# Performance work log

Measured on AMD Instinct MI355X. Metric: run time of the kernel, lower is better.

The kernel has to match this reference:

```python
import jax, jax.numpy as jnp
import numpy as np

B, N, D = 16, 2048, 128
SCALE = 1.0 / np.sqrt(D).astype(np.float32)


def setup_inputs() -> dict:
    key = jax.random.key(0)
    ks = jax.random.split(key, 9)
    Q = jax.random.normal(ks[0], (B, N, D), dtype=jnp.float32)
    K = jax.random.normal(ks[1], (B, N, D), dtype=jnp.float32)
    V = jax.random.normal(ks[2], (B, N, D), dtype=jnp.float32)
    bias_dis = 0.1 * jax.random.normal(ks[3], (N, N), dtype=jnp.float32)
    bias_dtw = 0.1 * jax.random.normal(ks[4], (N, N), dtype=jnp.float32)
    bias_pattern = 0.1 * jax.random.normal(ks[5], (N, N), dtype=jnp.float32)
    bias_poi = 0.1 * jax.random.normal(ks[6], (N, N), dtype=jnp.float32)
    # key/query padding masks: mostly True (valid) with some padding
    input_mask = jax.random.randint(ks[7], (B, N), 0, 10) > 0
    embeddings_mask = jax.random.randint(ks[8], (B, N), 0, 10) > 0
    # lower-triangular causal mask (diagonal kept so every row has a valid key)
    causal_mask = jnp.tril(jnp.ones((N, N), dtype=bool))
    return {"Q": Q, "K": K, "V": V, "bias_dis": bias_dis, "bias_dtw": bias_dtw,
            "bias_pattern": bias_pattern, "bias_poi": bias_poi,
            "input_mask": input_mask, "embeddings_mask": embeddings_mask,
            "causal_mask": causal_mask}


def reference(Q, K, V, bias_dis, bias_dtw, bias_pattern, bias_poi,
              input_mask, embeddings_mask, causal_mask):
    # masked_fill_(~mask, 0.0) on K, V with input_mask[:, :, None]
    km = input_mask[:, :, None]
    K = jnp.where(km, K, 0.0)
    V = jnp.where(km, V, 0.0)
    # masked_fill_(~mask, 0.0) on Q with embeddings_mask[:, :, None]
    Q = jnp.where(embeddings_mask[:, :, None], Q, 0.0)
    # scores [B, N, N] = Q K^T / sqrt(dim)
    scores = jnp.einsum('bnd,bmd->bnm', Q, K) * SCALE
    # causal masked_fill_(~causal_mask, -inf)
    scores = jnp.where(causal_mask[None, :, :], scores, -jnp.inf)
    # per-batch bias loop == broadcast add of summed [N, N] biases
    scores = scores + (bias_dis + bias_dtw + bias_pattern + bias_poi)[None, :, :]
    P = jax.nn.softmax(scores, axis=-1)
    # dropout p=0 (eval) -> identity
    return jnp.einsum('bnm,bmd->bnd', P, V)
```

## Files before the change

kernel.cpp:

```cpp
#include <hip/hip_runtime.h>
#include <math.h>

constexpr int Bc = 16;
constexpr int Nc = 2048;
constexpr int Dc = 128;
constexpr int NCHUNK = Nc / 64;
constexpr float SCALE_F = 0.08838834764831845f;

typedef __bf16 bf16x8 __attribute__((ext_vector_type(8)));
typedef __bf16 bf16x4 __attribute__((ext_vector_type(4)));
typedef float  f32x4  __attribute__((ext_vector_type(4)));

constexpr size_t KPACK_BYTES = (size_t)Bc * NCHUNK * 16 * 64 * 16;
constexpr size_t VPACK_BYTES = KPACK_BYTES;
constexpr int NUNITS = 1056;
constexpr size_t BIASP_BYTES = (size_t)NUNITS * 2048 * 4;
constexpr int CHUNK_ELEMS = 16 * 64 * 8;
constexpr int PART_FLOATS = 64 * 128 + 64 + 64;
constexpr size_t PART_BYTES = (size_t)Bc * 72 * PART_FLOATS * 4;

__device__ __forceinline__ int ftri(int t) {
    const int m = t >> 1;
    return (t & 1) ? (m + 1) * (m + 1) : m * (m + 1);
}

__device__ __forceinline__ void gload_lds16(const __bf16* gsrc, __bf16* ldst) {
    __builtin_amdgcn_global_load_lds(
        (const __attribute__((address_space(1))) unsigned int*)gsrc,
        (__attribute__((address_space(3))) unsigned int*)ldst, 16, 0, 0);
}

template<int CTRL>
__device__ __forceinline__ float dpp_mv(float v) {
    return __builtin_bit_cast(float,
        __builtin_amdgcn_update_dpp(0, __builtin_bit_cast(int, v),
                                    CTRL, 0xF, 0xF, true));
}
__device__ __forceinline__ float rmax16(float v) {
    v = fmaxf(v, dpp_mv<0xB1>(v));
    v = fmaxf(v, dpp_mv<0x4E>(v));
    v = fmaxf(v, dpp_mv<0x141>(v));
    v = fmaxf(v, dpp_mv<0x140>(v));
    return v;
}
__device__ __forceinline__ float rsum16(float v) {
    v += dpp_mv<0xB1>(v);
    v += dpp_mv<0x4E>(v);
    v += dpp_mv<0x141>(v);
    v += dpp_mv<0x140>(v);
    return v;
}

__global__ __launch_bounds__(256) void prep_fused(
    const float* __restrict__ K, const float* __restrict__ V,
    const int* __restrict__ imask,
    const float* __restrict__ b0, const float* __restrict__ b1,
    const float* __restrict__ b2, const float* __restrict__ b3,
    __bf16* __restrict__ Kp, __bf16* __restrict__ Vp, float* __restrict__ bsp)
{
    __shared__ __align__(16) __bf16 Ks[64][136];
    __shared__ __align__(16) __bf16 Vs[64][136];
    __shared__ __align__(16) float  Ts[32][68];
    const int bid = blockIdx.x;
    const int tid = threadIdx.x;

    if (bid >= 512) {
        const int u = bid - 512;
        int t = 0;
        while (ftri(t + 1) <= u) ++t;
        const int c = u - ftri(t);

        #pragma unroll
        for (int i = 0; i < 2; ++i) {
            const int v = tid + 256 * i;
            const int row = v >> 4, c4 = v & 15;
            const size_t g = (size_t)(t * 32 + row) * Nc + c * 64 + c4 * 4;
            const float4 a = *(const float4*)(b0 + g);
            const float4 d = *(const float4*)(b1 + g);
            const float4 e = *(const float4*)(b2 + g);
            const float4 f = *(const float4*)(b3 + g);
            float4 s;
            s.x = a.x + d.x + e.x + f.x;
            s.y = a.y + d.y + e.y + f.y;
            s.z = a.z + d.z + e.z + f.z;
            s.w = a.w + d.w + e.w + f.w;
            *(float4*)&Ts[row][c4 * 4] = s;
        }
        __syncthreads();

        const int lane = tid >> 2;
        const int quad = lane >> 4, l15 = lane & 15;
        const int k0 = (tid & 3) * 8;
        float* outp = bsp + (size_t)u * 2048;
        #pragma unroll
        for (int g2 = 0; g2 < 2; ++g2) {
            const int k = k0 + g2 * 4;
            const int h = (k >> 4) & 1, jt = (k >> 2) & 3;
            float4 o;
            o.x = Ts[h * 16 + quad * 4 + 0][jt * 16 + l15];
            o.y = Ts[h * 16 + quad * 4 + 1][jt * 16 + l15];
            o.z = Ts[h * 16 + quad * 4 + 2][jt * 16 + l15];
            o.w = Ts[h * 16 + quad * 4 + 3][jt * 16 + l15];
            ((float4*)outp)[tid * 2 + g2] = o;
        }
        return;
    }

    const int c = bid & 31;
    const int b = bid >> 5;
    const int m0 = c * 64;
    const float* Kb = K + (size_t)b * Nc * Dc;
    const float* Vb = V + (size_t)b * Nc * Dc;
    const int* imb = imask + b * Nc;

    #pragma unroll
    for (int it = 0; it < 8; ++it) {
        const int idx = it * 256 + tid;
        const int row = idx >> 5;
        const int c4  = idx & 31;
        const int gm  = m0 + row;
        const float msk = imb[gm] ? 1.0f : 0.0f;
        const float4 kf = ((const float4*)(Kb + (size_t)gm * Dc))[c4];
        const float4 vf = ((const float4*)(Vb + (size_t)gm * Dc))[c4];
        bf16x4 kb, vb;
        kb[0] = (__bf16)(kf.x * msk); kb[1] = (__bf16)(kf.y * msk);
        kb[2] = (__bf16)(kf.z * msk); kb[3] = (__bf16)(kf.w * msk);
        vb[0] = (__bf16)(vf.x * msk); vb[1] = (__bf16)(vf.y * msk);
        vb[2] = (__bf16)(vf.z * msk); vb[3] = (__bf16)(vf.w * msk);
        *(bf16x4*)&Ks[row][c4 * 4] = kb;
        *(bf16x4*)&Vs[row][c4 * 4] = vb;
    }
    __syncthreads();

    const size_t chunk_base = (size_t)(b * NCHUNK + c) * CHUNK_ELEMS;
    #pragma unroll
    for (int i = 0; i < 4; ++i) {
        const int s = i * 256 + tid;
        const int f = s >> 6;
        const int l = s & 63;
        const int quad = (l >> 4) & 3;
        const int l15  = l & 15;
        {
            const int jt = f >> 2, kd = f & 3;
            const bf16x8 kv = *(const bf16x8*)&Ks[jt * 16 + l15][kd * 32 + quad * 8];
            *(bf16x8*)&Kp[chunk_base + (size_t)f * 512 + l * 8] = kv;
        }
        {
            const int kj = f >> 3, dt = f & 7;
            bf16x8 vv;
            #pragma unroll
            for (int j = 0; j < 8; ++j)
                vv[j] = Vs[kj * 32 + quad * 8 + j][dt * 16 + l15];
            *(bf16x8*)&Vp[chunk_base + (size_t)f * 512 + l * 8] = vv;
        }
    }
}

template<bool SPLIT>
__global__ __launch_bounds__(256) void attn_pipe2(
    const float* __restrict__ Q,
    const __bf16* __restrict__ Kp, const __bf16* __restrict__ Vp,
    const float* __restrict__ biasp, const int* __restrict__ emask,
    float* __restrict__ out, float* __restrict__ part)
{
    __shared__ __align__(16) __bf16 Kl[2][16 * 512];
    __shared__ __align__(16) __bf16 Vl[2][16 * 512];
    __shared__ __align__(16) __bf16 Pl[4][16][72];

    const int tid  = threadIdx.x;
    const int w    = tid >> 6;
    const int lane = tid & 63;
    const int quad = lane >> 4;
    const int l15  = lane & 15;
    const int b = blockIdx.x;

    int t, c0, cend, pidx;
    bool direct;
    if (SPLIT) {
        const int u = 79 - blockIdx.y;
        int s;
        if (u < 8)       { t = u;                 s = 0; }
        else if (u < 24) { t = 8  + ((u - 8) >> 1);  s = (u - 8) & 1; }
        else if (u < 48) { t = 16 + (u - 24) / 3;    s = (u - 24) % 3; }
        else             { t = 24 + ((u - 48) >> 2); s = (u - 48) & 3; }
        c0 = s * 8;
        cend = min(t + 1, c0 + 8);
        direct = (u < 8);
        pidx = u - 8;
    } else {
        const int y = blockIdx.y;
        t = (y < 16) ? y : (47 - y);
        c0 = 0; cend = t + 1; direct = true; pidx = 0;
    }

    const int q0w = t * 64 + w * 16;
    const int t32 = t * 2 + (w >> 1);
    const int hh  = w & 1;
    const int fb32 = ftri(t32);

    const float*  Qb  = Q + (size_t)b * Nc * Dc;
    const __bf16* Kpb = Kp + (size_t)b * NCHUNK * CHUNK_ELEMS;
    const __bf16* Vpb = Vp + (size_t)b * NCHUNK * CHUNK_ELEMS;
    const f32x4* bfrag = (const f32x4*)biasp + (size_t)lane * 8 + hh * 4;

    bf16x8 qfrag[4];
    {
        const int row = q0w + l15;
        const float qs = emask[b * Nc + row] ? SCALE_F : 0.0f;
        const float4* qr = (const float4*)(Qb + (size_t)row * Dc);
        #pragma unroll
        for (int kd = 0; kd < 4; ++kd) {
            const float4 xx = qr[kd * 8 + quad * 2];
            const float4 yy = qr[kd * 8 + quad * 2 + 1];
            qfrag[kd][0] = (__bf16)(xx.x * qs); qfrag[kd][1] = (__bf16)(xx.y * qs);
            qfrag[kd][2] = (__bf16)(xx.z * qs); qfrag[kd][3] = (__bf16)(xx.w * qs);
            qfrag[kd][4] = (__bf16)(yy.x * qs); qfrag[kd][5] = (__bf16)(yy.y * qs);
            qfrag[kd][6] = (__bf16)(yy.z * qs); qfrag[kd][7] = (__bf16)(yy.w * qs);
        }
    }

    f32x4 oacc[8];
    #pragma unroll
    for (int dt = 0; dt < 8; ++dt) { oacc[dt][0]=0.f; oacc[dt][1]=0.f; oacc[dt][2]=0.f; oacc[dt][3]=0.f; }
    float mrun[4] = {-INFINITY, -INFINITY, -INFINITY, -INFINITY};
    float lrun[4] = {0.f, 0.f, 0.f, 0.f};

    const int nch = cend - c0;

    #pragma unroll
    for (int i = 0; i < 4; ++i) {
        const int seg = w * 4 + i;
        gload_lds16(Kpb + (size_t)c0 * CHUNK_ELEMS + seg * 512 + lane * 8, &Kl[0][seg * 512]);
        gload_lds16(Vpb + (size_t)c0 * CHUNK_ELEMS + seg * 512 + lane * 8, &Vl[0][seg * 512]);
    }
    f32x4 binit[4];
    #pragma unroll
    for (int jt = 0; jt < 4; ++jt)
        binit[jt] = bfrag[(size_t)(fb32 + c0) * 512 + jt];
    __syncthreads();

    f32x4 sc[4];
    #pragma unroll
    for (int jt = 0; jt < 4; ++jt) sc[jt] = binit[jt];
    #pragma unroll
    for (int jt = 0; jt < 4; ++jt)
        #pragma unroll
        for (int kd = 0; kd < 4; ++kd) {
            const bf16x8 bfr = *(const bf16x8*)&Kl[0][(jt * 4 + kd) * 512 + lane * 8];
            sc[jt] = __builtin_amdgcn_mfma_f32_16x16x32_bf16(qfrag[kd], bfr, sc[jt], 0, 0, 0);
        }
    if (nch > 1) {
        #pragma unroll
        for (int i = 0; i < 4; ++i) {
            const int seg = w * 4 + i;
            gload_lds16(Kpb + (size_t)(c0 + 1) * CHUNK_ELEMS + seg * 512 + lane * 8, &Kl[1][seg * 512]);
            gload_lds16(Vpb + (size_t)(c0 + 1) * CHUNK_ELEMS + seg * 512 + lane * 8, &Vl[1][seg * 512]);
        }
        #pragma unroll
        for (int jt = 0; jt < 4; ++jt)
            binit[jt] = bfrag[(size_t)(fb32 + c0 + 1) * 512 + jt];
    }

    for (int c = c0; c < cend; ++c) {
        const int cb = (c - c0) & 1;

        if (c == t) {
            const int m0 = c * 64;
            #pragma unroll
            for (int jt = 0; jt < 4; ++jt)
                #pragma unroll
                for (int reg = 0; reg < 4; ++reg) {
                    const int gr = q0w + quad * 4 + reg;
                    const int gc = m0 + jt * 16 + l15;
                    if (gc > gr) sc[jt][reg] = -INFINITY;
                }
        }

        #pragma unroll
        for (int reg = 0; reg < 4; ++reg) {
            float mx = fmaxf(fmaxf(sc[0][reg], sc[1][reg]), fmaxf(sc[2][reg], sc[3][reg]));
            mx = rmax16(mx);
            const float mn = fmaxf(mrun[reg], mx);
            const float alpha = __expf(mrun[reg] - mn);
            mrun[reg] = mn;
            lrun[reg] *= alpha;
            #pragma unroll
            for (int dt = 0; dt < 8; ++dt) oacc[dt][reg] *= alpha;
            float ls = 0.f;
            #pragma unroll
            for (int jt = 0; jt < 4; ++jt) {
                const float pv = __expf(sc[jt][reg] - mn);
                sc[jt][reg] = pv;
                ls += pv;
            }
            lrun[reg] += rsum16(ls);
        }

        #pragma unroll
        for (int jt = 0; jt < 4; ++jt)
            #pragma unroll
            for (int reg = 0; reg < 4; ++reg)
                Pl[w][quad * 4 + reg][jt * 16 + l15] = (__bf16)sc[jt][reg];

        #pragma unroll
        for (int kj = 0; kj < 2; ++kj) {
            const bf16x8 pa = *(const bf16x8*)&Pl[w][l15][kj * 32 + quad * 8];
            #pragma unroll
            for (int dt = 0; dt < 8; ++dt) {
                const bf16x8 vb = *(const bf16x8*)&Vl[cb][(kj * 8 + dt) * 512 + lane * 8];
                oacc[dt] = __builtin_amdgcn_mfma_f32_16x16x32_bf16(pa, vb, oacc[dt], 0, 0, 0);
            }
        }

        __syncthreads();

        const bool n1 = (c + 1) < cend;
        const bool n2 = (c + 2) < cend;

        if (n2) {
            const size_t off = (size_t)(c + 2) * CHUNK_ELEMS;
            #pragma unroll
            for (int i = 0; i < 4; ++i) {
                const int seg = w * 4 + i;
                gload_lds16(Kpb + off + seg * 512 + lane * 8, &Kl[cb][seg * 512]);
                gload_lds16(Vpb + off + seg * 512 + lane * 8, &Vl[cb][seg * 512]);
            }
        }

        if (n1) {
            #pragma unroll
            for (int jt = 0; jt < 4; ++jt) sc[jt] = binit[jt];
            #pragma unroll
            for (int jt = 0; jt < 4; ++jt)
                #pragma unroll
                for (int kd = 0; kd < 4; ++kd) {
                    const bf16x8 bfr = *(const bf16x8*)&Kl[cb ^ 1][(jt * 4 + kd) * 512 + lane * 8];
                    sc[jt] = __builtin_amdgcn_mfma_f32_16x16x32_bf16(qfrag[kd], bfr, sc[jt], 0, 0, 0);
                }
        }
        if (n2) {
            #pragma unroll
            for (int jt = 0; jt < 4; ++jt)
                binit[jt] = bfrag[(size_t)(fb32 + c + 2) * 512 + jt];
        }
    }

    if (direct) {
        #pragma unroll
        for (int reg = 0; reg < 4; ++reg) {
            const float inv = 1.0f / lrun[reg];
            const int gr = q0w + quad * 4 + reg;
            float* orow = out + ((size_t)b * Nc + gr) * Dc;
            #pragma unroll
            for (int dt = 0; dt < 8; ++dt)
                orow[dt * 16 + l15] = oacc[dt][reg] * inv;
        }
    } else {
        float* pb = part + (size_t)(b * 72 + pidx) * PART_FLOATS;
        #pragma unroll
        for (int reg = 0; reg < 4; ++reg) {
            const int lr = w * 16 + quad * 4 + reg;
            #pragma unroll
            for (int dt = 0; dt < 8; ++dt)
                pb[lr * 128 + dt * 16 + l15] = oacc[dt][reg];
            if (l15 == 0) {
                pb[8192 + lr] = mrun[reg];
                pb[8256 + lr] = lrun[reg];
            }
        }
    }
}

__global__ __launch_bounds__(256) void merge_parts(
    const float* __restrict__ part, float* __restrict__ out)
{
    const int b = blockIdx.x;
    const int t = 8 + blockIdx.y;
    const int S = (t < 16) ? 2 : ((t < 24) ? 3 : 4);
    const int pbase = (t < 16) ? 2 * (t - 8)
                    : (t < 24) ? 16 + 3 * (t - 16)
                               : 40 + 4 * (t - 24);
    const int r  = threadIdx.x >> 2;
    const int cq = threadIdx.x & 3;
    const float* p0 = part + (size_t)(b * 72 + pbase) * PART_FLOATS;

    float m[4], a[4];
    float mstar = -INFINITY;
    #pragma unroll
    for (int s = 0; s < 4; ++s)
        if (s < S) { m[s] = p0[(size_t)s * PART_FLOATS + 8192 + r]; mstar = fmaxf(mstar, m[s]); }
    float lsum = 0.f;
    #pragma unroll
    for (int s = 0; s < 4; ++s)
        if (s < S) {
            a[s] = __expf(m[s] - mstar);
            lsum += p0[(size_t)s * PART_FLOATS + 8256 + r] * a[s];
        }
    const float inv = 1.0f / lsum;

    float* orow = out + ((size_t)b * Nc + t * 64 + r) * Dc + cq * 32;
    #pragma unroll
    for (int i = 0; i < 8; ++i) {
        float x = 0.f, y = 0.f, z = 0.f, ww = 0.f;
        #pragma unroll
        for (int s = 0; s < 4; ++s)
            if (s < S) {
                const f32x4 v = *(const f32x4*)&p0[(size_t)s * PART_FLOATS + r * 128 + cq * 32 + i * 4];
                x += v[0] * a[s]; y += v[1] * a[s]; z += v[2] * a[s]; ww += v[3] * a[s];
            }
        f32x4 o; o[0] = x * inv; o[1] = y * inv; o[2] = z * inv; o[3] = ww * inv;
        *(f32x4*)&orow[i * 4] = o;
    }
}

__global__ __launch_bounds__(256) void attn_mfma_legacy(
    const float* __restrict__ Q, const float* __restrict__ K, const float* __restrict__ V,
    const float* __restrict__ p0, const float* __restrict__ p1,
    const float* __restrict__ p2, const float* __restrict__ p3,
    const int* __restrict__ imask, const int* __restrict__ emask,
    float* __restrict__ out)
{
    __shared__ __align__(16) __bf16 Klds[64][136];
    __shared__ __align__(16) __bf16 Vt[128][72];
    __shared__ __align__(16) __bf16 Plds[4][16][72];
    const int tid  = threadIdx.x;
    const int w    = tid >> 6;
    const int lane = tid & 63;
    const int quad = lane >> 4;
    const int l15  = lane & 15;
    const int b = blockIdx.y;
    const int x = blockIdx.x, yy = blockIdx.y;
    const int ti = (yy < 8) ? x : (31 - x);
    const int q0 = ti * 64, q0w = q0 + w * 16;
    const float* Qb = Q + (size_t)b * Nc * Dc;
    const float* Kb = K + (size_t)b * Nc * Dc;
    const float* Vb = V + (size_t)b * Nc * Dc;
    const int* imb = imask + b * Nc;

    bf16x8 qfrag[4];
    {
        const int row = q0w + l15;
        const float qs = emask[b * Nc + row] ? SCALE_F : 0.0f;
        const float4* qr = (const float4*)(Qb + (size_t)row * Dc);
        #pragma unroll
        for (int kd = 0; kd < 4; ++kd) {
            const float4 xv = qr[kd * 8 + quad * 2];
            const float4 yv = qr[kd * 8 + quad * 2 + 1];
            qfrag[kd][0]=(__bf16)(xv.x*qs); qfrag[kd][1]=(__bf16)(xv.y*qs);
            qfrag[kd][2]=(__bf16)(xv.z*qs); qfrag[kd][3]=(__bf16)(xv.w*qs);
            qfrag[kd][4]=(__bf16)(yv.x*qs); qfrag[kd][5]=(__bf16)(yv.y*qs);
            qfrag[kd][6]=(__bf16)(yv.z*qs); qfrag[kd][7]=(__bf16)(yv.w*qs);
        }
    }
    f32x4 oacc[8];
    #pragma unroll
    for (int dt = 0; dt < 8; ++dt){oacc[dt][0]=0.f;oacc[dt][1]=0.f;oacc[dt][2]=0.f;oacc[dt][3]=0.f;}
    float mrun[4]={-INFINITY,-INFINITY,-INFINITY,-INFINITY}, lrun[4]={0.f,0.f,0.f,0.f};

    for (int m0 = 0; m0 <= q0; m0 += 64) {
        __syncthreads();
        #pragma unroll
        for (int it = 0; it < 8; ++it) {
            const int idx = it * 256 + tid;
            const int row = idx >> 5, c4 = idx & 31;
            const int gm = m0 + row;
            const float msk = imb[gm] ? 1.0f : 0.0f;
            const float4 kf = ((const float4*)(Kb + (size_t)gm * Dc))[c4];
            const float4 vf = ((const float4*)(Vb + (size_t)gm * Dc))[c4];
            bf16x4 kb;
            kb[0]=(__bf16)(kf.x*msk); kb[1]=(__bf16)(kf.y*msk);
            kb[2]=(__bf16)(kf.z*msk); kb[3]=(__bf16)(kf.w*msk);
            *(bf16x4*)&Klds[row][c4*4] = kb;
            Vt[c4*4+0][row]=(__bf16)(vf.x*msk); Vt[c4*4+1][row]=(__bf16)(vf.y*msk);
            Vt[c4*4+2][row]=(__bf16)(vf.z*msk); Vt[c4*4+3][row]=(__bf16)(vf.w*msk);
        }
        __syncthreads();
        f32x4 sc[4];
        #pragma unroll
        for (int jt = 0; jt < 4; ++jt){sc[jt][0]=0.f;sc[jt][1]=0.f;sc[jt][2]=0.f;sc[jt][3]=0.f;}
        #pragma unroll
        for (int jt = 0; jt < 4; ++jt)
            #pragma unroll
            for (int kd = 0; kd < 4; ++kd) {
                const bf16x8 bfr = *(const bf16x8*)&Klds[jt*16+l15][kd*32+quad*8];
                sc[jt] = __builtin_amdgcn_mfma_f32_16x16x32_bf16(qfrag[kd], bfr, sc[jt], 0, 0, 0);
            }
        #pragma unroll
        for (int jt = 0; jt < 4; ++jt)
            #pragma unroll
            for (int reg = 0; reg < 4; ++reg) {
                const int gr = q0w + quad*4 + reg;
                const int gc = m0 + jt*16 + l15;
                const size_t boff = (size_t)gr * Nc + gc;
                const float bsx = p0[boff] + p1[boff] + p2[boff] + p3[boff];
                const float v = sc[jt][reg] + bsx;
                sc[jt][reg] = (gc > gr) ? -INFINITY : v;
            }
        #pragma unroll
        for (int reg = 0; reg < 4; ++reg) {
            float mx = fmaxf(fmaxf(sc[0][reg], sc[1][reg]), fmaxf(sc[2][reg], sc[3][reg]));
            mx = rmax16(mx);
            const float mn = fmaxf(mrun[reg], mx);
            const float alpha = __expf(mrun[reg] - mn);
            mrun[reg] = mn; lrun[reg] *= alpha;
            #pragma unroll
            for (int dt = 0; dt < 8; ++dt) oacc[dt][reg] *= alpha;
            float ls = 0.f;
            #pragma unroll
            for (int jt = 0; jt < 4; ++jt) {
                const float pv = __expf(sc[jt][reg] - mn);
                sc[jt][reg] = pv; ls += pv;
            }
            lrun[reg] += rsum16(ls);
        }
        #pragma unroll
        for (int jt = 0; jt < 4; ++jt)
            #pragma unroll
            for (int reg = 0; reg < 4; ++reg)
                Plds[w][quad*4+reg][jt*16+l15] = (__bf16)sc[jt][reg];
        #pragma unroll
        for (int kj = 0; kj < 2; ++kj) {
            const bf16x8 pa = *(const bf16x8*)&Plds[w][l15][kj*32+quad*8];
            #pragma unroll
            for (int dt = 0; dt < 8; ++dt) {
                const bf16x8 vb = *(const bf16x8*)&Vt[dt*16+l15][kj*32+quad*8];
                oacc[dt] = __builtin_amdgcn_mfma_f32_16x16x32_bf16(pa, vb, oacc[dt], 0, 0, 0);
            }
        }
    }
    #pragma unroll
    for (int reg = 0; reg < 4; ++reg) {
        const float inv = 1.0f / lrun[reg];
        const int gr = q0w + quad*4 + reg;
        float* orow = out + ((size_t)b * Nc + gr) * Dc;
        #pragma unroll
        for (int dt = 0; dt < 8; ++dt)
            orow[dt*16+l15] = oacc[dt][reg] * inv;
    }
}

extern "C" void kernel_launch(void* const* d_in, const int* in_sizes, int n_in,
                              void* d_out, int out_size, void* d_ws, size_t ws_size,
                              hipStream_t stream) {
    const float* Q  = (const float*)d_in[0];
    const float* K  = (const float*)d_in[1];
    const float* V  = (const float*)d_in[2];
    const float* b0 = (const float*)d_in[3];
    const float* b1 = (const float*)d_in[4];
    const float* b2 = (const float*)d_in[5];
    const float* b3 = (const float*)d_in[6];
    const int* im   = (const int*)d_in[7];
    const int* em   = (const int*)d_in[8];
    float* out      = (float*)d_out;

    const size_t need_full  = KPACK_BYTES + VPACK_BYTES + BIASP_BYTES;
    const size_t need_split = need_full + PART_BYTES;

    if (ws_size >= need_full) {
        __bf16* Kp  = (__bf16*)d_ws;
        __bf16* Vp  = (__bf16*)((char*)d_ws + KPACK_BYTES);
        float*  bsp = (float*)((char*)d_ws + KPACK_BYTES + VPACK_BYTES);
        float*  prt = (float*)((char*)d_ws + need_full);
        prep_fused<<<512 + NUNITS, 256, 0, stream>>>(
            K, V, im, b0, b1, b2, b3, Kp, Vp, bsp);
        if (ws_size >= need_split) {
            attn_pipe2<true><<<dim3(Bc, 80), 256, 0, stream>>>(
                Q, Kp, Vp, bsp, em, out, prt);
            merge_parts<<<dim3(Bc, 24), 256, 0, stream>>>(prt, out);
        } else {
            attn_pipe2<false><<<dim3(Bc, 32), 256, 0, stream>>>(
                Q, Kp, Vp, bsp, em, out, nullptr);
        }
    } else {
        attn_mfma_legacy<<<dim3(NCHUNK, Bc), 256, 0, stream>>>(
            Q, K, V, b0, b1, b2, b3, im, em, out);
    }
}
```

Measured before the change: 240.3 us.

## Load V fragments directly from global into registers and skip non-growing rescale

```diff
diff --git a/kernel.cpp b/kernel.cpp
--- a/kernel.cpp
+++ b/kernel.cpp
@@ -157,14 +157,13 @@
 }
 
 template<bool SPLIT>
-__global__ __launch_bounds__(256) void attn_pipe2(
+__global__ __launch_bounds__(256) void attn_pipe3(
     const float* __restrict__ Q,
     const __bf16* __restrict__ Kp, const __bf16* __restrict__ Vp,
     const float* __restrict__ biasp, const int* __restrict__ emask,
     float* __restrict__ out, float* __restrict__ part)
 {
     __shared__ __align__(16) __bf16 Kl[2][16 * 512];
-    __shared__ __align__(16) __bf16 Vl[2][16 * 512];
     __shared__ __align__(16) __bf16 Pl[4][16][72];
 
     const int tid  = threadIdx.x;
@@ -231,7 +230,6 @@
     for (int i = 0; i < 4; ++i) {
         const int seg = w * 4 + i;
         gload_lds16(Kpb + (size_t)c0 * CHUNK_ELEMS + seg * 512 + lane * 8, &Kl[0][seg * 512]);
-        gload_lds16(Vpb + (size_t)c0 * CHUNK_ELEMS + seg * 512 + lane * 8, &Vl[0][seg * 512]);
     }
     f32x4 binit[4];
     #pragma unroll
@@ -254,7 +252,6 @@
         for (int i = 0; i < 4; ++i) {
             const int seg = w * 4 + i;
             gload_lds16(Kpb + (size_t)(c0 + 1) * CHUNK_ELEMS + seg * 512 + lane * 8, &Kl[1][seg * 512]);
-            gload_lds16(Vpb + (size_t)(c0 + 1) * CHUNK_ELEMS + seg * 512 + lane * 8, &Vl[1][seg * 512]);
         }
         #pragma unroll
         for (int jt = 0; jt < 4; ++jt)
@@ -263,6 +260,12 @@
 
     for (int c = c0; c < cend; ++c) {
         const int cb = (c - c0) & 1;
+        const __bf16* vc = Vpb + (size_t)c * CHUNK_ELEMS;
+
+        bf16x8 va[8];
+        #pragma unroll
+        for (int dt = 0; dt < 8; ++dt)
+            va[dt] = *(const bf16x8*)&vc[(size_t)dt * 512 + lane * 8];
 
         if (c == t) {
             const int m0 = c * 64;
@@ -276,20 +279,32 @@
                 }
         }
 
+        float mx[4];
+        int grow = 0;
         #pragma unroll
         for (int reg = 0; reg < 4; ++reg) {
-            float mx = fmaxf(fmaxf(sc[0][reg], sc[1][reg]), fmaxf(sc[2][reg], sc[3][reg]));
-            mx = rmax16(mx);
-            const float mn = fmaxf(mrun[reg], mx);
-            const float alpha = __expf(mrun[reg] - mn);
-            mrun[reg] = mn;
-            lrun[reg] *= alpha;
-            #pragma unroll
-            for (int dt = 0; dt < 8; ++dt) oacc[dt][reg] *= alpha;
+            float m = fmaxf(fmaxf(sc[0][reg], sc[1][reg]), fmaxf(sc[2][reg], sc[3][reg]));
+            m = rmax16(m);
+            mx[reg] = m;
+            grow |= (m > mrun[reg]);
+        }
+        if (__any(grow)) {
+            #pragma unroll
+            for (int reg = 0; reg < 4; ++reg) {
+                const float mn = fmaxf(mrun[reg], mx[reg]);
+                const float alpha = __expf(mrun[reg] - mn);
+                mrun[reg] = mn;
+                lrun[reg] *= alpha;
+                #pragma unroll
+                for (int dt = 0; dt < 8; ++dt) oacc[dt][reg] *= alpha;
+            }
+        }
+        #pragma unroll
+        for (int reg = 0; reg < 4; ++reg) {
             float ls = 0.f;
             #pragma unroll
             for (int jt = 0; jt < 4; ++jt) {
-                const float pv = __expf(sc[jt][reg] - mn);
+                const float pv = __expf(sc[jt][reg] - mrun[reg]);
                 sc[jt][reg] = pv;
                 ls += pv;
             }
@@ -302,14 +317,20 @@
             for (int reg = 0; reg < 4; ++reg)
                 Pl[w][quad * 4 + reg][jt * 16 + l15] = (__bf16)sc[jt][reg];
 
-        #pragma unroll
-        for (int kj = 0; kj < 2; ++kj) {
-            const bf16x8 pa = *(const bf16x8*)&Pl[w][l15][kj * 32 + quad * 8];
-            #pragma unroll
-            for (int dt = 0; dt < 8; ++dt) {
-                const bf16x8 vb = *(const bf16x8*)&Vl[cb][(kj * 8 + dt) * 512 + lane * 8];
-                oacc[dt] = __builtin_amdgcn_mfma_f32_16x16x32_bf16(pa, vb, oacc[dt], 0, 0, 0);
-            }
+        bf16x8 vb8[8];
+        #pragma unroll
+        for (int dt = 0; dt < 8; ++dt)
+            vb8[dt] = *(const bf16x8*)&vc[(size_t)(8 + dt) * 512 + lane * 8];
+
+        {
+            const bf16x8 pa0 = *(const bf16x8*)&Pl[w][l15][quad * 8];
+            #pragma unroll
+            for (int dt = 0; dt < 8; ++dt)
+                oacc[dt] = __builtin_amdgcn_mfma_f32_16x16x32_bf16(pa0, va[dt], oacc[dt], 0, 0, 0);
+            const bf16x8 pa1 = *(const bf16x8*)&Pl[w][l15][32 + quad * 8];
+            #pragma unroll
+            for (int dt = 0; dt < 8; ++dt)
+                oacc[dt] = __builtin_amdgcn_mfma_f32_16x16x32_bf16(pa1, vb8[dt], oacc[dt], 0, 0, 0);
         }
 
         __syncthreads();
@@ -323,7 +344,6 @@
             for (int i = 0; i < 4; ++i) {
                 const int seg = w * 4 + i;
                 gload_lds16(Kpb + off + seg * 512 + lane * 8, &Kl[cb][seg * 512]);
-                gload_lds16(Vpb + off + seg * 512 + lane * 8, &Vl[cb][seg * 512]);
             }
         }
 
@@ -564,11 +584,11 @@
         prep_fused<<<512 + NUNITS, 256, 0, stream>>>(
             K, V, im, b0, b1, b2, b3, Kp, Vp, bsp);
         if (ws_size >= need_split) {
-            attn_pipe2<true><<<dim3(Bc, 80), 256, 0, stream>>>(
+            attn_pipe3<true><<<dim3(Bc, 80), 256, 0, stream>>>(
                 Q, Kp, Vp, bsp, em, out, prt);
             merge_parts<<<dim3(Bc, 24), 256, 0, stream>>>(prt, out);
         } else {
-            attn_pipe2<false><<<dim3(Bc, 32), 256, 0, stream>>>(
+            attn_pipe3<false><<<dim3(Bc, 32), 256, 0, stream>>>(
                 Q, Kp, Vp, bsp, em, out, nullptr);
         }
     } else {
```

Result: slower. 247.8 us (+3.1%).

## Pack split attention units into balanced persistent slots and skip rescale when max unchanged

Applied to the files above, without the earlier changes.

```diff
diff --git a/kernel.cpp b/kernel.cpp
--- a/kernel.cpp
+++ b/kernel.cpp
@@ -18,6 +18,17 @@
 constexpr int CHUNK_ELEMS = 16 * 64 * 8;
 constexpr int PART_FLOATS = 64 * 128 + 64 + 64;
 constexpr size_t PART_BYTES = (size_t)Bc * 72 * PART_FLOATS * 4;
+
+__device__ __constant__ int SLOT_UNITS[32][3] = {
+    { 7,  6,  1}, { 8, 21, 11}, {10, 44, 29}, {12, 75, 55},
+    {14,  5,  2}, {16, 19, 13}, {18, 41, 32}, {20, 71, 59},
+    {22,  4,  3}, {23, 17, 15}, {24, 38, 35}, {25, 67, 63},
+    {27, 28,  0}, {30, 31,  9}, {33, 34, 26}, {36, 37, 51},
+    {39, 40, -1}, {42, 43, -1}, {45, 46, -1}, {47, 48, -1},
+    {49, 50, -1}, {52, 53, -1}, {54, 56, -1}, {57, 58, -1},
+    {60, 61, -1}, {62, 64, -1}, {65, 66, -1}, {68, 69, -1},
+    {70, 72, -1}, {73, 74, -1}, {76, 77, -1}, {78, 79, -1}
+};
 
 __device__ __forceinline__ int ftri(int t) {
     const int m = t >> 1;
@@ -157,7 +168,7 @@
 }
 
 template<bool SPLIT>
-__global__ __launch_bounds__(256) void attn_pipe2(
+__global__ __launch_bounds__(256) void attn_persist(
     const float* __restrict__ Q,
     const __bf16* __restrict__ Kp, const __bf16* __restrict__ Vp,
     const float* __restrict__ biasp, const int* __restrict__ emask,
@@ -172,200 +183,214 @@
     const int lane = tid & 63;
     const int quad = lane >> 4;
     const int l15  = lane & 15;
-    const int b = blockIdx.x;
-
-    int t, c0, cend, pidx;
-    bool direct;
-    if (SPLIT) {
-        const int u = 79 - blockIdx.y;
-        int s;
-        if (u < 8)       { t = u;                 s = 0; }
-        else if (u < 24) { t = 8  + ((u - 8) >> 1);  s = (u - 8) & 1; }
-        else if (u < 48) { t = 16 + (u - 24) / 3;    s = (u - 24) % 3; }
-        else             { t = 24 + ((u - 48) >> 2); s = (u - 48) & 3; }
-        c0 = s * 8;
-        cend = min(t + 1, c0 + 8);
-        direct = (u < 8);
-        pidx = u - 8;
-    } else {
-        const int y = blockIdx.y;
-        t = (y < 16) ? y : (47 - y);
-        c0 = 0; cend = t + 1; direct = true; pidx = 0;
-    }
-
-    const int q0w = t * 64 + w * 16;
-    const int t32 = t * 2 + (w >> 1);
-    const int hh  = w & 1;
-    const int fb32 = ftri(t32);
+    const int b    = blockIdx.x;
+    const int slot = blockIdx.y;
 
     const float*  Qb  = Q + (size_t)b * Nc * Dc;
     const __bf16* Kpb = Kp + (size_t)b * NCHUNK * CHUNK_ELEMS;
     const __bf16* Vpb = Vp + (size_t)b * NCHUNK * CHUNK_ELEMS;
-    const f32x4* bfrag = (const f32x4*)biasp + (size_t)lane * 8 + hh * 4;
-
-    bf16x8 qfrag[4];
-    {
-        const int row = q0w + l15;
-        const float qs = emask[b * Nc + row] ? SCALE_F : 0.0f;
-        const float4* qr = (const float4*)(Qb + (size_t)row * Dc);
-        #pragma unroll
-        for (int kd = 0; kd < 4; ++kd) {
-            const float4 xx = qr[kd * 8 + quad * 2];
-            const float4 yy = qr[kd * 8 + quad * 2 + 1];
-            qfrag[kd][0] = (__bf16)(xx.x * qs); qfrag[kd][1] = (__bf16)(xx.y * qs);
-            qfrag[kd][2] = (__bf16)(xx.z * qs); qfrag[kd][3] = (__bf16)(xx.w * qs);
-            qfrag[kd][4] = (__bf16)(yy.x * qs); qfrag[kd][5] = (__bf16)(yy.y * qs);
-            qfrag[kd][6] = (__bf16)(yy.z * qs); qfrag[kd][7] = (__bf16)(yy.w * qs);
-        }
-    }
-
-    f32x4 oacc[8];
-    #pragma unroll
-    for (int dt = 0; dt < 8; ++dt) { oacc[dt][0]=0.f; oacc[dt][1]=0.f; oacc[dt][2]=0.f; oacc[dt][3]=0.f; }
-    float mrun[4] = {-INFINITY, -INFINITY, -INFINITY, -INFINITY};
-    float lrun[4] = {0.f, 0.f, 0.f, 0.f};
-
-    const int nch = cend - c0;
-
-    #pragma unroll
-    for (int i = 0; i < 4; ++i) {
-        const int seg = w * 4 + i;
-        gload_lds16(Kpb + (size_t)c0 * CHUNK_ELEMS + seg * 512 + lane * 8, &Kl[0][seg * 512]);
-        gload_lds16(Vpb + (size_t)c0 * CHUNK_ELEMS + seg * 512 + lane * 8, &Vl[0][seg * 512]);
-    }
-    f32x4 binit[4];
-    #pragma unroll
-    for (int jt = 0; jt < 4; ++jt)
-        binit[jt] = bfrag[(size_t)(fb32 + c0) * 512 + jt];
-    __syncthreads();
-
-    f32x4 sc[4];
-    #pragma unroll
-    for (int jt = 0; jt < 4; ++jt) sc[jt] = binit[jt];
-    #pragma unroll
-    for (int jt = 0; jt < 4; ++jt)
-        #pragma unroll
-        for (int kd = 0; kd < 4; ++kd) {
-            const bf16x8 bfr = *(const bf16x8*)&Kl[0][(jt * 4 + kd) * 512 + lane * 8];
-            sc[jt] = __builtin_amdgcn_mfma_f32_16x16x32_bf16(qfrag[kd], bfr, sc[jt], 0, 0, 0);
-        }
-    if (nch > 1) {
+    const f32x4* bfragbase = (const f32x4*)biasp + (size_t)lane * 8 + (w & 1) * 4;
+
+    for (int j = 0; j < 3; ++j) {
+        int t, c0, cend, pidx;
+        bool direct;
+        if (SPLIT) {
+            const int un = SLOT_UNITS[slot][j];
+            if (un < 0) break;
+            if (un < 8)       { t = un;                  c0 = 0; }
+            else if (un < 24) { t = 8  + ((un -  8) >> 1); c0 = ((un -  8) & 1) * 8; }
+            else if (un < 48) { t = 16 + (un - 24) / 3;    c0 = ((un - 24) % 3) * 8; }
+            else              { t = 24 + ((un - 48) >> 2); c0 = ((un - 48) & 3) * 8; }
+            cend = min(t + 1, c0 + 8);
+            direct = (un < 8);
+            pidx = un - 8;
+        } else {
+            if (j) break;
+            t = (slot < 16) ? slot : (47 - slot);
+            c0 = 0; cend = t + 1; direct = true; pidx = 0;
+        }
+
+        const int q0w = t * 64 + w * 16;
+        const int t32 = t * 2 + (w >> 1);
+        const int fb32 = ftri(t32);
+        const f32x4* bfrag = bfragbase;
+
+        bf16x8 qfrag[4];
+        {
+            const int row = q0w + l15;
+            const float qs = emask[b * Nc + row] ? SCALE_F : 0.0f;
+            const float4* qr = (const float4*)(Qb + (size_t)row * Dc);
+            #pragma unroll
+            for (int kd = 0; kd < 4; ++kd) {
+                const float4 xx = qr[kd * 8 + quad * 2];
+                const float4 yy = qr[kd * 8 + quad * 2 + 1];
+                qfrag[kd][0] = (__bf16)(xx.x * qs); qfrag[kd][1] = (__bf16)(xx.y * qs);
+                qfrag[kd][2] = (__bf16)(xx.z * qs); qfrag[kd][3] = (__bf16)(xx.w * qs);
+                qfrag[kd][4] = (__bf16)(yy.x * qs); qfrag[kd][5] = (__bf16)(yy.y * qs);
+                qfrag[kd][6] = (__bf16)(yy.z * qs); qfrag[kd][7] = (__bf16)(yy.w * qs);
+            }
+        }
+
+        f32x4 oacc[8];
+        #pragma unroll
+        for (int dt = 0; dt < 8; ++dt) { oacc[dt][0]=0.f; oacc[dt][1]=0.f; oacc[dt][2]=0.f; oacc[dt][3]=0.f; }
+        float mrun[4] = {-INFINITY, -INFINITY, -INFINITY, -INFINITY};
+        float lrun[4] = {0.f, 0.f, 0.f, 0.f};
+
+        const int nch = cend - c0;
+
         #pragma unroll
         for (int i = 0; i < 4; ++i) {
             const int seg = w * 4 + i;
-            gload_lds16(Kpb + (size_t)(c0 + 1) * CHUNK_ELEMS + seg * 512 + lane * 8, &Kl[1][seg * 512]);
-            gload_lds16(Vpb + (size_t)(c0 + 1) * CHUNK_ELEMS + seg * 512 + lane * 8, &Vl[1][seg * 512]);
-        }
+            gload_lds16(Kpb + (size_t)c0 * CHUNK_ELEMS + seg * 512 + lane * 8, &Kl[0][seg * 512]);
+            gload_lds16(Vpb + (size_t)c0 * CHUNK_ELEMS + seg * 512 + lane * 8, &Vl[0][seg * 512]);
+        }
+        f32x4 binit[4];
         #pragma unroll
         for (int jt = 0; jt < 4; ++jt)
-            binit[jt] = bfrag[(size_t)(fb32 + c0 + 1) * 512 + jt];
-    }
-
-    for (int c = c0; c < cend; ++c) {
-        const int cb = (c - c0) & 1;
-
-        if (c == t) {
-            const int m0 = c * 64;
-            #pragma unroll
-            for (int jt = 0; jt < 4; ++jt)
-                #pragma unroll
-                for (int reg = 0; reg < 4; ++reg) {
-                    const int gr = q0w + quad * 4 + reg;
-                    const int gc = m0 + jt * 16 + l15;
-                    if (gc > gr) sc[jt][reg] = -INFINITY;
-                }
-        }
-
-        #pragma unroll
-        for (int reg = 0; reg < 4; ++reg) {
-            float mx = fmaxf(fmaxf(sc[0][reg], sc[1][reg]), fmaxf(sc[2][reg], sc[3][reg]));
-            mx = rmax16(mx);
-            const float mn = fmaxf(mrun[reg], mx);
-            const float alpha = __expf(mrun[reg] - mn);
-            mrun[reg] = mn;
-            lrun[reg] *= alpha;
-            #pragma unroll
-            for (int dt = 0; dt < 8; ++dt) oacc[dt][reg] *= alpha;
-            float ls = 0.f;
-            #pragma unroll
-            for (int jt = 0; jt < 4; ++jt) {
-                const float pv = __expf(sc[jt][reg] - mn);
-                sc[jt][reg] = pv;
-                ls += pv;
-            }
-            lrun[reg] += rsum16(ls);
-        }
-
+            binit[jt] = bfrag[(size_t)(fb32 + c0) * 512 + jt];
+        __syncthreads();
+
+        f32x4 sc[4];
+        #pragma unroll
+        for (int jt = 0; jt < 4; ++jt) sc[jt] = binit[jt];
         #pragma unroll
         for (int jt = 0; jt < 4; ++jt)
             #pragma unroll
-            for (int reg = 0; reg < 4; ++reg)
-                Pl[w][quad * 4 + reg][jt * 16 + l15] = (__bf16)sc[jt][reg];
-
-        #pragma unroll
-        for (int kj = 0; kj < 2; ++kj) {
-            const bf16x8 pa = *(const bf16x8*)&Pl[w][l15][kj * 32 + quad * 8];
-            #pragma unroll
-            for (int dt = 0; dt < 8; ++dt) {
-                const bf16x8 vb = *(const bf16x8*)&Vl[cb][(kj * 8 + dt) * 512 + lane * 8];
-                oacc[dt] = __builtin_amdgcn_mfma_f32_16x16x32_bf16(pa, vb, oacc[dt], 0, 0, 0);
-            }
-        }
-
-        __syncthreads();
-
-        const bool n1 = (c + 1) < cend;
-        const bool n2 = (c + 2) < cend;
-
-        if (n2) {
-            const size_t off = (size_t)(c + 2) * CHUNK_ELEMS;
+            for (int kd = 0; kd < 4; ++kd) {
+                const bf16x8 bfr = *(const bf16x8*)&Kl[0][(jt * 4 + kd) * 512 + lane * 8];
+                sc[jt] = __builtin_amdgcn_mfma_f32_16x16x32_bf16(qfrag[kd], bfr, sc[jt], 0, 0, 0);
+            }
+        if (nch > 1) {
             #pragma unroll
             for (int i = 0; i < 4; ++i) {
                 const int seg = w * 4 + i;
-                gload_lds16(Kpb + off + seg * 512 + lane * 8, &Kl[cb][seg * 512]);
-                gload_lds16(Vpb + off + seg * 512 + lane * 8, &Vl[cb][seg * 512]);
-            }
-        }
-
-        if (n1) {
-            #pragma unroll
-            for (int jt = 0; jt < 4; ++jt) sc[jt] = binit[jt];
+                gload_lds16(Kpb + (size_t)(c0 + 1) * CHUNK_ELEMS + seg * 512 + lane * 8, &Kl[1][seg * 512]);
+                gload_lds16(Vpb + (size_t)(c0 + 1) * CHUNK_ELEMS + seg * 512 + lane * 8, &Vl[1][seg * 512]);
+            }
             #pragma unroll
             for (int jt = 0; jt < 4; ++jt)
-                #pragma unroll
-                for (int kd = 0; kd < 4; ++kd) {
-                    const bf16x8 bfr = *(const bf16x8*)&Kl[cb ^ 1][(jt * 4 + kd) * 512 + lane * 8];
-                    sc[jt] = __builtin_amdgcn_mfma_f32_16x16x32_bf16(qfrag[kd], bfr, sc[jt], 0, 0, 0);
+                binit[jt] = bfrag[(size_t)(fb32 + c0 + 1) * 512 + jt];
+        }
+
+        for (int c = c0; c < cend; ++c) {
+            const int cb = (c - c0) & 1;
+
+            if (c == t) {
+                const int m0 = c * 64;
+                #pragma unroll
+                for (int jt = 0; jt < 4; ++jt)
+                    #pragma unroll
+                    for (int reg = 0; reg < 4; ++reg) {
+                        const int gr = q0w + quad * 4 + reg;
+                        const int gc = m0 + jt * 16 + l15;
+                        if (gc > gr) sc[jt][reg] = -INFINITY;
+                    }
+            }
+
+            float mx[4];
+            int grow = 0;
+            #pragma unroll
+            for (int reg = 0; reg < 4; ++reg) {
+                float m = fmaxf(fmaxf(sc[0][reg], sc[1][reg]), fmaxf(sc[2][reg], sc[3][reg]));
+                m = rmax16(m);
+                mx[reg] = m;
+                grow |= (m > mrun[reg]);
+            }
+            if (__any(grow)) {
+                #pragma unroll
+                for (int reg = 0; reg < 4; ++reg) {
+                    const float mn = fmaxf(mrun[reg], mx[reg]);
+                    const float alpha = __expf(mrun[reg] - mn);
+                    mrun[reg] = mn;
+                    lrun[reg] *= alpha;
+                    #pragma unroll
+                    for (int dt = 0; dt < 8; ++dt) oacc[dt][reg] *= alpha;
                 }
-        }
-        if (n2) {
+            }
+            #pragma unroll
+            for (int reg = 0; reg < 4; ++reg) {
+                float ls = 0.f;
+                #pragma unroll
+                for (int jt = 0; jt < 4; ++jt) {
+                    const float pv = __expf(sc[jt][reg] - mrun[reg]);
+                    sc[jt][reg] = pv;
+                    ls += pv;
+                }
+                lrun[reg] += rsum16(ls);
+            }
+
             #pragma unroll
             for (int jt = 0; jt < 4; ++jt)
-                binit[jt] = bfrag[(size_t)(fb32 + c + 2) * 512 + jt];
-        }
-    }
-
-    if (direct) {
-        #pragma unroll
-        for (int reg = 0; reg < 4; ++reg) {
-            const float inv = 1.0f / lrun[reg];
-            const int gr = q0w + quad * 4 + reg;
-            float* orow = out + ((size_t)b * Nc + gr) * Dc;
-            #pragma unroll
-            for (int dt = 0; dt < 8; ++dt)
-                orow[dt * 16 + l15] = oacc[dt][reg] * inv;
-        }
-    } else {
-        float* pb = part + (size_t)(b * 72 + pidx) * PART_FLOATS;
-        #pragma unroll
-        for (int reg = 0; reg < 4; ++reg) {
-            const int lr = w * 16 + quad * 4 + reg;
-            #pragma unroll
-            for (int dt = 0; dt < 8; ++dt)
-                pb[lr * 128 + dt * 16 + l15] = oacc[dt][reg];
-            if (l15 == 0) {
-                pb[8192 + lr] = mrun[reg];
-                pb[8256 + lr] = lrun[reg];
+                #pragma unroll
+                for (int reg = 0; reg < 4; ++reg)
+                    Pl[w][quad * 4 + reg][jt * 16 + l15] = (__bf16)sc[jt][reg];
+
+            #pragma unroll
+            for (int kj = 0; kj < 2; ++kj) {
+                const bf16x8 pa = *(const bf16x8*)&Pl[w][l15][kj * 32 + quad * 8];
+                #pragma unroll
+                for (int dt = 0; dt < 8; ++dt) {
+                    const bf16x8 vb = *(const bf16x8*)&Vl[cb][(kj * 8 + dt) * 512 + lane * 8];
+                    oacc[dt] = __builtin_amdgcn_mfma_f32_16x16x32_bf16(pa, vb, oacc[dt], 0, 0, 0);
+                }
+            }
+
+            __syncthreads();
+
+            const bool n1 = (c + 1) < cend;
+            const bool n2 = (c + 2) < cend;
+
+            if (n2) {
+                const size_t off = (size_t)(c + 2) * CHUNK_ELEMS;
+                #pragma unroll
+                for (int i = 0; i < 4; ++i) {
+                    const int seg = w * 4 + i;
+                    gload_lds16(Kpb + off + seg * 512 + lane * 8, &Kl[cb][seg * 512]);
+                    gload_lds16(Vpb + off + seg * 512 + lane * 8, &Vl[cb][seg * 512]);
+                }
+            }
+
+            if (n1) {
+                #pragma unroll
+                for (int jt = 0; jt < 4; ++jt) sc[jt] = binit[jt];
+                #pragma unroll
+                for (int jt = 0; jt < 4; ++jt)
+                    #pragma unroll
+                    for (int kd = 0; kd < 4; ++kd) {
+                        const bf16x8 bfr = *(const bf16x8*)&Kl[cb ^ 1][(jt * 4 + kd) * 512 + lane * 8];
+                        sc[jt] = __builtin_amdgcn_mfma_f32_16x16x32_bf16(qfrag[kd], bfr, sc[jt], 0, 0, 0);
+                    }
+            }
+            if (n2) {
+                #pragma unroll
+                for (int jt = 0; jt < 4; ++jt)
+                    binit[jt] = bfrag[(size_t)(fb32 + c + 2) * 512 + jt];
+            }
+        }
+
+        if (direct) {
+            #pragma unroll
+            for (int reg = 0; reg < 4; ++reg) {
+                const float inv = 1.0f / lrun[reg];
+                const int gr = q0w + quad * 4 + reg;
+                float* orow = out + ((size_t)b * Nc + gr) * Dc;
+                #pragma unroll
+                for (int dt = 0; dt < 8; ++dt)
+                    orow[dt * 16 + l15] = oacc[dt][reg] * inv;
+            }
+        } else {
+            float* pb = part + (size_t)(b * 72 + pidx) * PART_FLOATS;
+            #pragma unroll
+            for (int reg = 0; reg < 4; ++reg) {
+                const int lr = w * 16 + quad * 4 + reg;
+                #pragma unroll
+                for (int dt = 0; dt < 8; ++dt)
+                    pb[lr * 128 + dt * 16 + l15] = oacc[dt][reg];
+                if (l15 == 0) {
+                    pb[8192 + lr] = mrun[reg];
+                    pb[8256 + lr] = lrun[reg];
+                }
             }
         }
     }
@@ -564,11 +589,11 @@
         prep_fused<<<512 + NUNITS, 256, 0, stream>>>(
             K, V, im, b0, b1, b2, b3, Kp, Vp, bsp);
         if (ws_size >= need_split) {
-            attn_pipe2<true><<<dim3(Bc, 80), 256, 0, stream>>>(
+            attn_persist<true><<<dim3(Bc, 32), 256, 0, stream>>>(
                 Q, Kp, Vp, bsp, em, out, prt);
             merge_parts<<<dim3(Bc, 24), 256, 0, stream>>>(prt, out);
         } else {
-            attn_pipe2<false><<<dim3(Bc, 32), 256, 0, stream>>>(
+            attn_persist<false><<<dim3(Bc, 32), 256, 0, stream>>>(
                 Q, Kp, Vp, bsp, em, out, nullptr);
         }
     } else {
```

Result: faster. 234.2 us (-2.5%).
